# Performance work log

Measured on AMD Instinct MI355X. Metric: run time of the kernel, lower is better.

## Reference

```python
import jax, jax.numpy as jnp
import numpy as np

N_NODES = 50000
N_EDGES = 800000
HIDDEN = 64


def _init_linear(key, fan_in, fan_out):
    kw, kb = jax.random.split(key)
    lim = 1.0 / np.sqrt(fan_in)
    W = jax.random.uniform(kw, (fan_in, fan_out), jnp.float32, -lim, lim)
    b = jax.random.uniform(kb, (fan_out,), jnp.float32, -lim, lim)
    return W, b


def setup_inputs() -> dict:
    key = jax.random.key(0)
    ks = jax.random.split(key, 10)
    feat = jax.random.normal(ks[0], (N_NODES, HIDDEN), jnp.float32)
    x = jax.random.normal(ks[1], (N_NODES, 3), jnp.float32)
    src = jax.random.randint(ks[2], (N_EDGES,), 0, N_NODES, jnp.int32)
    dst = jax.random.randint(ks[3], (N_EDGES,), 0, N_NODES, jnp.int32)
    # message MLP: (2H+1) -> H -> H, relu after both layers (last_activation=mid)
    W1, b1 = _init_linear(ks[4], 2 * HIDDEN + 1, HIDDEN)
    W2, b2 = _init_linear(ks[5], HIDDEN, HIDDEN)
    # soft edge gate: H -> 1
    we, be = _init_linear(ks[6], HIDDEN, 1)
    # update MLP: H -> H -> H, relu mid, no last activation
    U1, c1 = _init_linear(ks[7], HIDDEN, HIDDEN)
    U2, c2 = _init_linear(ks[8], HIDDEN, HIDDEN)
    return dict(feat=feat, x=x, src=src, dst=dst,
                W1=W1, b1=b1, W2=W2, b2=b2, we=we, be=be,
                U1=U1, c1=c1, U2=U2, c2=c2)


def reference(feat, x, src, dst, W1, b1, W2, b2, we, be, U1, c1, U2, c2):
    # per-edge squared distance between endpoint coordinates: [E, 1]
    sqd = jnp.sum((x[src] - x[dst]) ** 2, axis=-1, keepdims=True)
    # message input: [E, 2H+1]
    msg_in = jnp.concatenate([feat[src], feat[dst], sqd], axis=-1)
    # 2-layer message MLP with relu mid and last activation
    m = jax.nn.relu(jax.nn.relu(msg_in @ W1 + b1) @ W2 + b2)
    # sigmoid soft-edge gate: [E, 1]
    gate = jax.nn.sigmoid(m @ we + be)
    # scatter-sum gated messages to destination nodes: [N, H]
    m_sum = jax.ops.segment_sum(m * gate, dst, num_segments=N_NODES)
    # node update MLP on (m_sum + feat), residual add
    h = m_sum + feat
    h_new = jax.nn.relu(h @ U1 + c1) @ U2 + c2
    return h_new + feat
```

## Files before the change

### kernel.cpp

```cpp
#include <hip/hip_runtime.h>
#include <hip/hip_bf16.h>
#include <stdint.h>

#define N_NODES 50000
#define N_EDGES 800000
#define HDIM 64
#define SCAN_N (N_NODES + 1)

#define MSUM_OFF   0
#define EP_OFF     12800000
#define DEG_OFF    (EP_OFF + 12800000)
#define OFFS_OFF   (DEG_OFF + 204800)
#define POS_OFF    (OFFS_OFF + 204800)
#define FB_OFF     (POS_OFF + 204800)
#define W1T_OFF    (FB_OFF + (size_t)N_NODES * HDIM * 2)
#define W2T_OFF    (W1T_OFF + 16384)
#define U1T_OFF    (W2T_OFF + 8192)
#define U2T_OFF    (U1T_OFF + 8192)
#define CST_OFF    (U2T_OFF + 8192)
#define WS_NEED    (CST_OFF + 4096)

#define CVT_BLOCKS   1563
#define PREPW_BLOCKS 82
#define MZ_BLOCKS    3125
#define HIST_BLOCKS  1024

typedef __attribute__((ext_vector_type(8))) short short8;
typedef __attribute__((ext_vector_type(4))) float floatx4;

__device__ __forceinline__ float bf2f(unsigned short u) {
    union { unsigned int i; float f; } v; v.i = ((unsigned int)u) << 16; return v.f;
}
__device__ __forceinline__ unsigned short f2bf(float f) {
    __hip_bfloat16 h = __float2bfloat16(f);
    return *reinterpret_cast<unsigned short*>(&h);
}

__device__ __forceinline__ int detect_is_bf16(const unsigned short* p) {
    int cnt = 0;
    #pragma unroll
    for (int i = 0; i < 64; ++i) {
        unsigned short b = p[i];
        int e = (b >> 7) & 0xFF;
        cnt += ((e >= 97 && e <= 157) || (b & 0x7FFF) == 0) ? 1 : 0;
    }
    return cnt >= 56;
}

__device__ __forceinline__ float getf(const void* p, unsigned int i, int isb) {
    return isb ? bf2f(((const unsigned short*)p)[i]) : ((const float*)p)[i];
}

__device__ __forceinline__ short8 get8bf(const void* p, unsigned int i, int isb) {
    if (isb) {
        return *reinterpret_cast<const short8*>((const short*)p + i);
    } else {
        const float4 f0 = *reinterpret_cast<const float4*>((const float*)p + i);
        const float4 f1 = *reinterpret_cast<const float4*>((const float*)p + i + 4);
        short8 a;
        a[0] = (short)f2bf(f0.x); a[1] = (short)f2bf(f0.y);
        a[2] = (short)f2bf(f0.z); a[3] = (short)f2bf(f0.w);
        a[4] = (short)f2bf(f1.x); a[5] = (short)f2bf(f1.y);
        a[6] = (short)f2bf(f1.z); a[7] = (short)f2bf(f1.w);
        return a;
    }
}

#define COMPILER_FENCE() asm volatile("" ::: "memory")
#define WAIT_LDS() __builtin_amdgcn_s_waitcnt(0xC07F)

__global__ __launch_bounds__(256) void prep_kernel(
    const void* __restrict__ feat, unsigned short* __restrict__ fb,
    const void* __restrict__ W1, const void* __restrict__ W2,
    const void* __restrict__ U1, const void* __restrict__ U2,
    const void* __restrict__ b1, const void* __restrict__ b2,
    const void* __restrict__ we, const void* __restrict__ be,
    unsigned short* __restrict__ w1t, unsigned short* __restrict__ w2t,
    unsigned short* __restrict__ u1t, unsigned short* __restrict__ u2t,
    float* __restrict__ cst,
    const int* __restrict__ dst, int* __restrict__ deg,
    uint4* __restrict__ msumz)
{
    const int b = blockIdx.x;
    if (b < CVT_BLOCKS) {
        const int isb = detect_is_bf16((const unsigned short*)feat);
        int i = (b * 256 + threadIdx.x) * 8;
        if (i >= N_NODES * HDIM) return;
        if (isb) {
            *reinterpret_cast<uint4*>(fb + i) =
                *reinterpret_cast<const uint4*>((const unsigned short*)feat + i);
        } else {
            float4 f0 = *reinterpret_cast<const float4*>((const float*)feat + i);
            float4 f1 = *reinterpret_cast<const float4*>((const float*)feat + i + 4);
            ushort4 a = {f2bf(f0.x), f2bf(f0.y), f2bf(f0.z), f2bf(f0.w)};
            ushort4 c = {f2bf(f1.x), f2bf(f1.y), f2bf(f1.z), f2bf(f1.w)};
            *reinterpret_cast<ushort4*>(fb + i)     = a;
            *reinterpret_cast<ushort4*>(fb + i + 4) = c;
        }
    } else if (b < CVT_BLOCKS + PREPW_BLOCKS) {
        const int isb = detect_is_bf16((const unsigned short*)feat);
        int idx = (b - CVT_BLOCKS) * 256 + threadIdx.x;
        if (idx < 8192) {
            int n = idx >> 7, k = idx & 127;
            w1t[idx] = f2bf(getf(W1, k * 64 + n, isb));
        } else if (idx < 12288) {
            int i = idx - 8192, n = i >> 6, k = i & 63;
            w2t[i] = f2bf(getf(W2, k * 64 + n, isb));
        } else if (idx < 16384) {
            int i = idx - 12288, n = i >> 6, k = i & 63;
            u1t[i] = f2bf(getf(U1, k * 64 + n, isb));
        } else if (idx < 20480) {
            int i = idx - 16384, n = i >> 6, k = i & 63;
            u2t[i] = f2bf(getf(U2, k * 64 + n, isb));
        } else if (idx < 20737) {
            int i = idx - 20480;
            float v;
            if (i < 64)       v = getf(b1, i, isb);
            else if (i < 128) v = getf(W1, 128 * 64 + (i - 64), isb);
            else if (i < 192) v = getf(b2, i - 128, isb);
            else if (i < 256) v = getf(we, i - 192, isb);
            else              v = getf(be, 0, isb);
            cst[i] = v;
        }
    } else if (b < CVT_BLOCKS + PREPW_BLOCKS + MZ_BLOCKS) {
        int i = (b - CVT_BLOCKS - PREPW_BLOCKS) * 256 + threadIdx.x;
        if (i < N_NODES * HDIM / 4)
            msumz[i] = (uint4){0u, 0u, 0u, 0u};
    } else {
        int e0 = (b - CVT_BLOCKS - PREPW_BLOCKS - MZ_BLOCKS) * 256 + threadIdx.x;
        for (int e = e0; e < N_EDGES; e += HIST_BLOCKS * 256)
            atomicAdd(&deg[dst[e]], 1);
    }
}

__global__ void scan1_kernel(const int* __restrict__ deg, int* __restrict__ part) {
    __shared__ int s[1024];
    int g = blockIdx.x * 1024 + threadIdx.x;
    s[threadIdx.x] = (g < SCAN_N) ? deg[g] : 0;
    __syncthreads();
    for (int off = 512; off > 0; off >>= 1) {
        if (threadIdx.x < off) s[threadIdx.x] += s[threadIdx.x + off];
        __syncthreads();
    }
    if (threadIdx.x == 0) part[blockIdx.x] = s[0];
}

__global__ void scan2_kernel(int* __restrict__ part, int nparts) {
    if (threadIdx.x == 0) {
        int run = 0;
        for (int i = 0; i < nparts; ++i) { int t = part[i]; part[i] = run; run += t; }
    }
}

__global__ void scan3_kernel(const int* __restrict__ deg, const int* __restrict__ part,
                             int* __restrict__ offs, int* __restrict__ pos) {
    __shared__ int s[1024];
    int g = blockIdx.x * 1024 + threadIdx.x;
    int v = (g < SCAN_N) ? deg[g] : 0;
    s[threadIdx.x] = v;
    __syncthreads();
    for (int off = 1; off < 1024; off <<= 1) {
        int t = (threadIdx.x >= off) ? s[threadIdx.x - off] : 0;
        __syncthreads();
        s[threadIdx.x] += t;
        __syncthreads();
    }
    int excl = s[threadIdx.x] - v + part[blockIdx.x];
    if (g < SCAN_N) { offs[g] = excl; pos[g] = excl; }
}

__global__ __launch_bounds__(256) void permute_kernel(
    const void* __restrict__ feat, const void* __restrict__ xpos,
    const int* __restrict__ src, const int* __restrict__ dst,
    int* __restrict__ pos, uint4* __restrict__ epack)
{
    const int isb = detect_is_bf16((const unsigned short*)feat);
    int e = blockIdx.x * 256 + threadIdx.x;
    if (e < N_EDGES) {
        int s = src[e], d = dst[e];
        int slot = atomicAdd(&pos[d], 1);
        float dx = getf(xpos, s * 3 + 0, isb) - getf(xpos, d * 3 + 0, isb);
        float dy = getf(xpos, s * 3 + 1, isb) - getf(xpos, d * 3 + 1, isb);
        float dz = getf(xpos, s * 3 + 2, isb) - getf(xpos, d * 3 + 2, isb);
        float sqd = dx * dx + dy * dy + dz * dz;
        uint4 p;
        p.x = (unsigned int)s;
        p.y = (unsigned int)d;
        p.z = __float_as_uint(sqd);
        p.w = 0u;
        epack[slot] = p;
    }
}

template <bool CSR>
__global__ __launch_bounds__(512, 4) void edge_kernel(
    const unsigned short* __restrict__ fbf,
    const unsigned short* __restrict__ w1t, const unsigned short* __restrict__ w2t,
    const float* __restrict__ cst,
    const void* __restrict__ feat, const void* __restrict__ xpos,
    const int* __restrict__ src, const int* __restrict__ dst,
    const uint4* __restrict__ epack,
    const void* __restrict__ W1, const void* __restrict__ b1,
    const void* __restrict__ W2, const void* __restrict__ b2,
    const void* __restrict__ we, const void* __restrict__ be,
    float* __restrict__ msum, unsigned int msum_cap)
{
    __shared__ __align__(16) short sW1[16][64][8];
    __shared__ __align__(16) short sW2[8][64][8];
    __shared__ __align__(16) short sA2[8][16][72];

    const int tid  = threadIdx.x;
    const int wave = tid >> 6;
    const int lane = tid & 63;
    const int l15  = lane & 15;
    const int quad = lane >> 4;
    const int rowb = quad * 4;

    float b1r[4], w1lr[4], b2r[4], wer[4];
    float ber;
    short8 bw1[4][4];
    short8 bw2[2][4];

    if constexpr (CSR) {
        for (int i = tid; i < 16 * 64; i += 512) {
            int f = i >> 6, l = i & 63;
            int n = (f & 3) * 16 + (l & 15);
            int k0 = (f >> 2) * 32 + (l >> 4) * 8;
            *reinterpret_cast<short8*>(&sW1[f][l][0]) =
                *reinterpret_cast<const short8*>(w1t + n * 128 + k0);
        }
        for (int i = tid; i < 8 * 64; i += 512) {
            int f = i >> 6, l = i & 63;
            int n = (f & 3) * 16 + (l & 15);
            int k0 = (f >> 2) * 32 + (l >> 4) * 8;
            *reinterpret_cast<short8*>(&sW2[f][l][0]) =
                *reinterpret_cast<const short8*>(w2t + n * 64 + k0);
        }
        #pragma unroll
        for (int nt = 0; nt < 4; ++nt) {
            int n = nt * 16 + l15;
            b1r[nt]  = cst[n];
            w1lr[nt] = cst[64 + n];
            b2r[nt]  = cst[128 + n];
            wer[nt]  = cst[192 + n];
        }
        ber = cst[256];
        __syncthreads();

        const int nbiter = N_EDGES / 256;
        for (int it = blockIdx.x; it < nbiter; it += gridDim.x) {
            const int ebase = it * 256 + wave * 16;

            int sidx = 0, didx = 0;
            float sqd = 0.f;
            if (lane < 32) {
                int e = ebase + l15 + ((lane >> 4) << 7);
                uint4 p = epack[e];
                sidx = (int)p.x;
                didx = (int)p.y;
                sqd  = __uint_as_float(p.z);
            }
            const int snA = __shfl(sidx, l15);
            const int dnA = __shfl(didx, l15);
            const int snB = __shfl(sidx, l15 + 16);
            const int dnB = __shfl(didx, l15 + 16);

            short8 caA[4], caB[4];
            #pragma unroll
            for (int c = 0; c < 4; ++c) {
                const int nA = (c < 2) ? snA : dnA;
                const int nB = (c < 2) ? snB : dnB;
                caA[c] = *reinterpret_cast<const short8*>(
                    (const short*)fbf + (unsigned int)nA * 64u + (c & 1) * 32 + quad * 8);
                caB[c] = *reinterpret_cast<const short8*>(
                    (const short*)fbf + (unsigned int)nB * 64u + (c & 1) * 32 + quad * 8);
            }

            floatx4 accA[4], accB[4];
            #pragma unroll
            for (int nt = 0; nt < 4; ++nt) {
                accA[nt] = (floatx4){0.f, 0.f, 0.f, 0.f};
                accB[nt] = (floatx4){0.f, 0.f, 0.f, 0.f};
            }
            #pragma unroll
            for (int c = 0; c < 4; ++c) {
                #pragma unroll
                for (int nt = 0; nt < 4; ++nt) {
                    short8 wb = *reinterpret_cast<const short8*>(&sW1[c * 4 + nt][lane][0]);
                    accA[nt] = __builtin_amdgcn_mfma_f32_16x16x32_bf16(caA[c], wb, accA[nt], 0, 0, 0);
                    accB[nt] = __builtin_amdgcn_mfma_f32_16x16x32_bf16(caB[c], wb, accB[nt], 0, 0, 0);
                }
            }

            float sqA[4], sqB[4];
            #pragma unroll
            for (int r = 0; r < 4; ++r) {
                sqA[r] = __shfl(sqd, rowb + r);
                sqB[r] = __shfl(sqd, 16 + rowb + r);
            }

            #pragma unroll
            for (int nt = 0; nt < 4; ++nt)
                #pragma unroll
                for (int r = 0; r < 4; ++r) {
                    float vA = fmaxf(fmaf(sqA[r], w1lr[nt], accA[nt][r]) + b1r[nt], 0.f);
                    sA2[wave][rowb + r][nt * 16 + l15] = (short)f2bf(vA);
                }
            COMPILER_FENCE();
            WAIT_LDS();

            floatx4 acc2A[4];
            #pragma unroll
            for (int nt = 0; nt < 4; ++nt) acc2A[nt] = (floatx4){0.f, 0.f, 0.f, 0.f};
            #pragma unroll
            for (int c = 0; c < 2; ++c) {
                short8 aA = *reinterpret_cast<const short8*>(&sA2[wave][l15][c * 32 + quad * 8]);
                #pragma unroll
                for (int nt = 0; nt < 4; ++nt) {
                    short8 wb = *reinterpret_cast<const short8*>(&sW2[c * 4 + nt][lane][0]);
                    acc2A[nt] = __builtin_amdgcn_mfma_f32_16x16x32_bf16(aA, wb, acc2A[nt], 0, 0, 0);
                }
            }
            COMPILER_FENCE();
            WAIT_LDS();

            #pragma unroll
            for (int nt = 0; nt < 4; ++nt)
                #pragma unroll
                for (int r = 0; r < 4; ++r) {
                    float vB = fmaxf(fmaf(sqB[r], w1lr[nt], accB[nt][r]) + b1r[nt], 0.f);
                    sA2[wave][rowb + r][nt * 16 + l15] = (short)f2bf(vB);
                }
            COMPILER_FENCE();
            WAIT_LDS();

            floatx4 acc2B[4];
            #pragma unroll
            for (int nt = 0; nt < 4; ++nt) acc2B[nt] = (floatx4){0.f, 0.f, 0.f, 0.f};
            #pragma unroll
            for (int c = 0; c < 2; ++c) {
                short8 aB = *reinterpret_cast<const short8*>(&sA2[wave][l15][c * 32 + quad * 8]);
                #pragma unroll
                for (int nt = 0; nt < 4; ++nt) {
                    short8 wb = *reinterpret_cast<const short8*>(&sW2[c * 4 + nt][lane][0]);
                    acc2B[nt] = __builtin_amdgcn_mfma_f32_16x16x32_bf16(aB, wb, acc2B[nt], 0, 0, 0);
                }
            }
            COMPILER_FENCE();

            float mvA[4][4], mvB[4][4];
            float pA[4] = {0.f, 0.f, 0.f, 0.f};
            float pB[4] = {0.f, 0.f, 0.f, 0.f};
            #pragma unroll
            for (int nt = 0; nt < 4; ++nt)
                #pragma unroll
                for (int r = 0; r < 4; ++r) {
                    float vA = fmaxf(acc2A[nt][r] + b2r[nt], 0.f);
                    float vB = fmaxf(acc2B[nt][r] + b2r[nt], 0.f);
                    mvA[nt][r] = vA;
                    mvB[nt][r] = vB;
                    pA[r] = fmaf(vA, wer[nt], pA[r]);
                    pB[r] = fmaf(vB, wer[nt], pB[r]);
                }
            #pragma unroll
            for (int off = 1; off < 16; off <<= 1)
                #pragma unroll
                for (int r = 0; r < 4; ++r) {
                    pA[r] += __shfl_xor(pA[r], off);
                    pB[r] += __shfl_xor(pB[r], off);
                }
            float gA[4], gB[4];
            #pragma unroll
            for (int r = 0; r < 4; ++r) {
                gA[r] = 1.f / (1.f + __expf(-(pA[r] + ber)));
                gB[r] = 1.f / (1.f + __expf(-(pB[r] + ber)));
            }

            int grp = (lane >> 4) & 1;
            int nd = __shfl(didx, grp * 16 + ((l15 + 1) & 15));
            int flag = (lane < 32) && ((l15 == 15) || (nd != didx));
            unsigned long long bal = __ballot(flag);
            unsigned int mA = (unsigned int)(bal & 0xFFFFull);
            unsigned int mB = (unsigned int)((bal >> 16) & 0xFFFFull);

            int lo = 0;
            while (mA) {
                int hi = __ffs(mA) - 1;
                float s0 = 0.f, s1 = 0.f, s2 = 0.f, s3 = 0.f;
                #pragma unroll
                for (int r = 0; r < 4; ++r) {
                    int gr = rowb + r;
                    float g = (gr >= lo && gr <= hi) ? gA[r] : 0.f;
                    s0 = fmaf(g, mvA[0][r], s0);
                    s1 = fmaf(g, mvA[1][r], s1);
                    s2 = fmaf(g, mvA[2][r], s2);
                    s3 = fmaf(g, mvA[3][r], s3);
                }
                s0 += __shfl_xor(s0, 16); s0 += __shfl_xor(s0, 32);
                s1 += __shfl_xor(s1, 16); s1 += __shfl_xor(s1, 32);
                s2 += __shfl_xor(s2, 16); s2 += __shfl_xor(s2, 32);
                s3 += __shfl_xor(s3, 16); s3 += __shfl_xor(s3, 32);
                int d = __shfl(didx, hi);
                float v = (quad == 0) ? s0 : (quad == 1) ? s1 : (quad == 2) ? s2 : s3;
                unsafeAtomicAdd(&msum[(unsigned int)d * 64u + (unsigned int)quad * 16u + l15], v);
                lo = hi + 1;
                mA &= mA - 1;
            }
            lo = 0;
            while (mB) {
                int hi = __ffs(mB) - 1;
                float s0 = 0.f, s1 = 0.f, s2 = 0.f, s3 = 0.f;
                #pragma unroll
                for (int r = 0; r < 4; ++r) {
                    int gr = rowb + r;
                    float g = (gr >= lo && gr <= hi) ? gB[r] : 0.f;
                    s0 = fmaf(g, mvB[0][r], s0);
                    s1 = fmaf(g, mvB[1][r], s1);
                    s2 = fmaf(g, mvB[2][r], s2);
                    s3 = fmaf(g, mvB[3][r], s3);
                }
                s0 += __shfl_xor(s0, 16); s0 += __shfl_xor(s0, 32);
                s1 += __shfl_xor(s1, 16); s1 += __shfl_xor(s1, 32);
                s2 += __shfl_xor(s2, 16); s2 += __shfl_xor(s2, 32);
                s3 += __shfl_xor(s3, 16); s3 += __shfl_xor(s3, 32);
                int d = __shfl(didx, 16 + hi);
                float v = (quad == 0) ? s0 : (quad == 1) ? s1 : (quad == 2) ? s2 : s3;
                unsafeAtomicAdd(&msum[(unsigned int)d * 64u + (unsigned int)quad * 16u + l15], v);
                lo = hi + 1;
                mB &= mB - 1;
            }
        }
    } else {
        const int isb = detect_is_bf16((const unsigned short*)feat);
        #pragma unroll
        for (int c = 0; c < 4; ++c)
            #pragma unroll
            for (int nt = 0; nt < 4; ++nt) {
                short8 b;
                #pragma unroll
                for (int j = 0; j < 8; ++j)
                    b[j] = (short)f2bf(getf(W1, (c * 32 + quad * 8 + j) * 64 + nt * 16 + l15, isb));
                bw1[c][nt] = b;
            }
        #pragma unroll
        for (int c = 0; c < 2; ++c)
            #pragma unroll
            for (int nt = 0; nt < 4; ++nt) {
                short8 b;
                #pragma unroll
                for (int j = 0; j < 8; ++j)
                    b[j] = (short)f2bf(getf(W2, (c * 32 + quad * 8 + j) * 64 + nt * 16 + l15, isb));
                bw2[c][nt] = b;
            }
        #pragma unroll
        for (int nt = 0; nt < 4; ++nt) {
            int n = nt * 16 + l15;
            b1r[nt]  = getf(b1, n, isb);
            w1lr[nt] = getf(W1, 128 * 64 + n, isb);
            b2r[nt]  = getf(b2, n, isb);
            wer[nt]  = getf(we, n, isb);
        }
        ber = getf(be, 0, isb);

        const int ntiles = N_EDGES / 128;
        for (int t = blockIdx.x; t < ntiles; t += gridDim.x) {
            const int ebase = t * 128 + wave * 16;
            int sidx = 0, didx = 0;
            float sqd = 0.f;
            if (lane < 16) {
                int e = ebase + lane;
                sidx = src[e];
                didx = dst[e];
                float dx = getf(xpos, sidx * 3 + 0, isb) - getf(xpos, didx * 3 + 0, isb);
                float dy = getf(xpos, sidx * 3 + 1, isb) - getf(xpos, didx * 3 + 1, isb);
                float dz = getf(xpos, sidx * 3 + 2, isb) - getf(xpos, didx * 3 + 2, isb);
                sqd = dx * dx + dy * dy + dz * dz;
            }
            const int sn     = __shfl(sidx, l15);
            const int dn_row = __shfl(didx, l15);

            floatx4 acc[4];
            #pragma unroll
            for (int nt = 0; nt < 4; ++nt) acc[nt] = (floatx4){0.f, 0.f, 0.f, 0.f};
            #pragma unroll
            for (int c = 0; c < 4; ++c) {
                const int node = (c < 2) ? sn : dn_row;
                const unsigned int aoff = (unsigned int)node * 64u + (c & 1) * 32 + quad * 8;
                short8 a = get8bf(feat, aoff, isb);
                #pragma unroll
                for (int nt = 0; nt < 4; ++nt)
                    acc[nt] = __builtin_amdgcn_mfma_f32_16x16x32_bf16(a, bw1[c][nt], acc[nt], 0, 0, 0);
            }

            float sq[4];
            #pragma unroll
            for (int r = 0; r < 4; ++r) sq[r] = __shfl(sqd, rowb + r);
            #pragma unroll
            for (int nt = 0; nt < 4; ++nt)
                #pragma unroll
                for (int r = 0; r < 4; ++r) {
                    float v = fmaxf(acc[nt][r] + b1r[nt] + sq[r] * w1lr[nt], 0.f);
                    sA2[wave][rowb + r][nt * 16 + l15] = (short)f2bf(v);
                }
            COMPILER_FENCE();
            WAIT_LDS();

            floatx4 acc2[4];
            #pragma unroll
            for (int nt = 0; nt < 4; ++nt) acc2[nt] = (floatx4){0.f, 0.f, 0.f, 0.f};
            #pragma unroll
            for (int c = 0; c < 2; ++c) {
                short8 a = *reinterpret_cast<const short8*>(&sA2[wave][l15][c * 32 + quad * 8]);
                #pragma unroll
                for (int nt = 0; nt < 4; ++nt)
                    acc2[nt] = __builtin_amdgcn_mfma_f32_16x16x32_bf16(a, bw2[c][nt], acc2[nt], 0, 0, 0);
            }
            COMPILER_FENCE();
            WAIT_LDS();

            float mval[4][4];
            float part[4] = {0.f, 0.f, 0.f, 0.f};
            #pragma unroll
            for (int nt = 0; nt < 4; ++nt)
                #pragma unroll
                for (int r = 0; r < 4; ++r) {
                    float v = fmaxf(acc2[nt][r] + b2r[nt], 0.f);
                    mval[nt][r] = v;
                    part[r] += v * wer[nt];
                }
            #pragma unroll
            for (int off = 1; off < 16; off <<= 1)
                #pragma unroll
                for (int r = 0; r < 4; ++r) part[r] += __shfl_xor(part[r], off);
            float gate[4];
            #pragma unroll
            for (int r = 0; r < 4; ++r)
                gate[r] = 1.f / (1.f + __expf(-(part[r] + ber)));

            #pragma unroll
            for (int r = 0; r < 4; ++r) {
                int dn = __shfl(didx, rowb + r);
                unsigned int base = (unsigned int)dn * 64u;
                if (base + 64u <= msum_cap) {
                    #pragma unroll
                    for (int nt = 0; nt < 4; ++nt)
                        unsafeAtomicAdd(&msum[base + nt * 16 + l15], mval[nt][r] * gate[r]);
                }
            }
        }
    }
}

__global__ __launch_bounds__(256, 2) void node_kernel(
    const float* __restrict__ msum,
    const unsigned short* __restrict__ u1t, const unsigned short* __restrict__ u2t,
    const void* __restrict__ feat,
    const void* __restrict__ U1, const void* __restrict__ c1v,
    const void* __restrict__ U2, const void* __restrict__ c2v,
    void* __restrict__ out)
{
    __shared__ __align__(16) short sT[4][16][72];
    __shared__ __align__(16) float sF[4][16][68];

    const int isb  = detect_is_bf16((const unsigned short*)feat);
    const int tid  = threadIdx.x;
    const int wave = tid >> 6;
    const int lane = tid & 63;
    const int l15  = lane & 15;
    const int quad = lane >> 4;

    short8 u1f[2][4], u2f[2][4];
    if (u1t) {
        #pragma unroll
        for (int nt = 0; nt < 4; ++nt) {
            const int n = nt * 16 + l15;
            #pragma unroll
            for (int c = 0; c < 2; ++c) {
                u1f[c][nt] = *reinterpret_cast<const short8*>(u1t + n * 64 + c * 32 + quad * 8);
                u2f[c][nt] = *reinterpret_cast<const short8*>(u2t + n * 64 + c * 32 + quad * 8);
            }
        }
    } else {
        #pragma unroll
        for (int c = 0; c < 2; ++c)
            #pragma unroll
            for (int nt = 0; nt < 4; ++nt) {
                short8 a, b;
                #pragma unroll
                for (int j = 0; j < 8; ++j) {
                    int k = c * 32 + quad * 8 + j, n = nt * 16 + l15;
                    a[j] = (short)f2bf(getf(U1, k * 64 + n, isb));
                    b[j] = (short)f2bf(getf(U2, k * 64 + n, isb));
                }
                u1f[c][nt] = a; u2f[c][nt] = b;
            }
    }
    float c1r[4], c2r[4];
    #pragma unroll
    for (int nt = 0; nt < 4; ++nt) {
        c1r[nt] = getf(c1v, nt * 16 + l15, isb);
        c2r[nt] = getf(c2v, nt * 16 + l15, isb);
    }
    const int rowb = quad * 4;

    const int ntile = (N_NODES + 15) / 16;
    const int t = blockIdx.x * 4 + wave;
    if (t < ntile) {
        const int node = t * 16 + l15;

        short8 ah[2];
        #pragma unroll
        for (int c = 0; c < 2; ++c) {
            unsigned int off = (unsigned int)node * 64u + c * 32 + quad * 8;
            float4 m0 = *reinterpret_cast<const float4*>(msum + off);
            float4 m1 = *reinterpret_cast<const float4*>(msum + off + 4);
            float mv[8] = {m0.x, m0.y, m0.z, m0.w, m1.x, m1.y, m1.z, m1.w};
            float hv[8];
            if (isb) {
                short8 fv = *reinterpret_cast<const short8*>((const short*)feat + off);
                #pragma unroll
                for (int j = 0; j < 8; ++j) hv[j] = bf2f((unsigned short)fv[j]);
            } else {
                float4 f0 = *reinterpret_cast<const float4*>((const float*)feat + off);
                float4 f1 = *reinterpret_cast<const float4*>((const float*)feat + off + 4);
                hv[0] = f0.x; hv[1] = f0.y; hv[2] = f0.z; hv[3] = f0.w;
                hv[4] = f1.x; hv[5] = f1.y; hv[6] = f1.z; hv[7] = f1.w;
            }
            short8 a;
            #pragma unroll
            for (int j = 0; j < 8; ++j) a[j] = (short)f2bf(mv[j] + hv[j]);
            ah[c] = a;
        }

        floatx4 acc[4];
        #pragma unroll
        for (int nt = 0; nt < 4; ++nt) acc[nt] = (floatx4){0.f, 0.f, 0.f, 0.f};
        #pragma unroll
        for (int c = 0; c < 2; ++c)
            #pragma unroll
            for (int nt = 0; nt < 4; ++nt)
                acc[nt] = __builtin_amdgcn_mfma_f32_16x16x32_bf16(ah[c], u1f[c][nt], acc[nt], 0, 0, 0);

        #pragma unroll
        for (int nt = 0; nt < 4; ++nt)
            #pragma unroll
            for (int r = 0; r < 4; ++r) {
                float v = fmaxf(acc[nt][r] + c1r[nt], 0.f);
                sT[wave][rowb + r][nt * 16 + l15] = (short)f2bf(v);
            }
        COMPILER_FENCE();
        WAIT_LDS();

        floatx4 acc2[4];
        #pragma unroll
        for (int nt = 0; nt < 4; ++nt) acc2[nt] = (floatx4){0.f, 0.f, 0.f, 0.f};
        #pragma unroll
        for (int c = 0; c < 2; ++c) {
            short8 a = *reinterpret_cast<const short8*>(&sT[wave][l15][c * 32 + quad * 8]);
            #pragma unroll
            for (int nt = 0; nt < 4; ++nt)
                acc2[nt] = __builtin_amdgcn_mfma_f32_16x16x32_bf16(a, u2f[c][nt], acc2[nt], 0, 0, 0);
        }
        COMPILER_FENCE();

        #pragma unroll
        for (int nt = 0; nt < 4; ++nt)
            #pragma unroll
            for (int r = 0; r < 4; ++r)
                sF[wave][rowb + r][nt * 16 + l15] = acc2[nt][r] + c2r[nt];
        COMPILER_FENCE();
        WAIT_LDS();

        const unsigned int ob = (unsigned int)node * 64u + quad * 16;
        if (isb) {
            const unsigned short* fp = (const unsigned short*)feat + ob;
            unsigned short* op = (unsigned short*)out + ob;
            #pragma unroll
            for (int k = 0; k < 2; ++k) {
                ushort4 o0, o1;
                float4 v0 = *reinterpret_cast<const float4*>(&sF[wave][l15][quad * 16 + k * 8]);
                float4 v1 = *reinterpret_cast<const float4*>(&sF[wave][l15][quad * 16 + k * 8 + 4]);
                const ushort4 f0 = *reinterpret_cast<const ushort4*>(fp + k * 8);
                const ushort4 f1 = *reinterpret_cast<const ushort4*>(fp + k * 8 + 4);
                o0.x = f2bf(v0.x + bf2f(f0.x)); o0.y = f2bf(v0.y + bf2f(f0.y));
                o0.z = f2bf(v0.z + bf2f(f0.z)); o0.w = f2bf(v0.w + bf2f(f0.w));
                o1.x = f2bf(v1.x + bf2f(f1.x)); o1.y = f2bf(v1.y + bf2f(f1.y));
                o1.z = f2bf(v1.z + bf2f(f1.z)); o1.w = f2bf(v1.w + bf2f(f1.w));
                *reinterpret_cast<ushort4*>(op + k * 8)     = o0;
                *reinterpret_cast<ushort4*>(op + k * 8 + 4) = o1;
            }
        } else {
            const float* fp = (const float*)feat + ob;
            float* op = (float*)out + ob;
            #pragma unroll
            for (int k = 0; k < 4; ++k) {
                float4 v = *reinterpret_cast<const float4*>(&sF[wave][l15][quad * 16 + k * 4]);
                float4 f = *reinterpret_cast<const float4*>(fp + k * 4);
                float4 o = {v.x + f.x, v.y + f.y, v.z + f.z, v.w + f.w};
                *reinterpret_cast<float4*>(op + k * 4) = o;
            }
        }
        COMPILER_FENCE();
    }
}

extern "C" void kernel_launch(void* const* d_in, const int* in_sizes, int n_in,
                              void* d_out, int out_size, void* d_ws, size_t ws_size,
                              hipStream_t stream) {
    const void* feat = d_in[0];
    const void* x    = d_in[1];
    const int* src   = (const int*)d_in[2];
    const int* dst   = (const int*)d_in[3];
    const void* W1   = d_in[4];
    const void* b1   = d_in[5];
    const void* W2   = d_in[6];
    const void* b2   = d_in[7];
    const void* we   = d_in[8];
    const void* be   = d_in[9];
    const void* U1   = d_in[10];
    const void* c1   = d_in[11];
    const void* U2   = d_in[12];
    const void* c2   = d_in[13];
    char* ws = (char*)d_ws;

    if (ws_size >= WS_NEED) {
        float* msum = (float*)(ws + MSUM_OFF);
        uint4* epack = (uint4*)(ws + EP_OFF);
        int* deg  = (int*)(ws + DEG_OFF);
        int* offs = (int*)(ws + OFFS_OFF);
        int* pos  = (int*)(ws + POS_OFF);
        unsigned short* fb  = (unsigned short*)(ws + FB_OFF);
        unsigned short* w1t = (unsigned short*)(ws + W1T_OFF);
        unsigned short* w2t = (unsigned short*)(ws + W2T_OFF);
        unsigned short* u1t = (unsigned short*)(ws + U1T_OFF);
        unsigned short* u2t = (unsigned short*)(ws + U2T_OFF);
        float* cst = (float*)(ws + CST_OFF);

        hipMemsetAsync(deg, 0, 204800, stream);
        prep_kernel<<<CVT_BLOCKS + PREPW_BLOCKS + MZ_BLOCKS + HIST_BLOCKS, 256, 0, stream>>>(
            feat, fb, W1, W2, U1, U2, b1, b2, we, be,
            w1t, w2t, u1t, u2t, cst, dst, deg, (uint4*)msum);
        scan1_kernel<<<49, 1024, 0, stream>>>(deg, offs + 51200 - 64);
        scan2_kernel<<<1, 64, 0, stream>>>(offs + 51200 - 64, 49);
        scan3_kernel<<<49, 1024, 0, stream>>>(deg, offs + 51200 - 64, offs, pos);
        permute_kernel<<<(N_EDGES + 255) / 256, 256, 0, stream>>>(feat, x, src, dst, pos, epack);
        edge_kernel<true><<<768, 512, 0, stream>>>(fb, w1t, w2t, cst, feat, x, src, dst, epack,
                                                   W1, b1, W2, b2, we, be,
                                                   msum, (unsigned int)(N_NODES * HDIM));
        node_kernel<<<((N_NODES + 15) / 16 + 3) / 4, 256, 0, stream>>>(
            msum, u1t, u2t, feat, U1, c1, U2, c2, d_out);
    } else {
        float* msum = (float*)ws;
        size_t need = (size_t)N_NODES * HDIM * sizeof(float);
        size_t clr  = need < ws_size ? need : ws_size;
        unsigned int cap = (unsigned int)(ws_size / sizeof(float));
        if (cap > (unsigned int)(N_NODES * HDIM)) cap = (unsigned int)(N_NODES * HDIM);

        hipMemsetAsync(msum, 0, clr, stream);
        edge_kernel<false><<<1250, 512, 0, stream>>>(nullptr, nullptr, nullptr, nullptr,
                                                     feat, x, src, dst,
                                                     nullptr, W1, b1, W2, b2, we, be,
                                                     msum, cap);
        node_kernel<<<((N_NODES + 15) / 16 + 3) / 4, 256, 0, stream>>>(
            msum, nullptr, nullptr, feat, U1, c1, U2, c2, d_out);
    }
}
```

Measured before the change: 268.8 us.

## Fold scan phases, memset msum, double-buffer LDS, use contiguous edge chunks per block

```diff
diff --git a/kernel.cpp b/kernel.cpp
--- a/kernel.cpp
+++ b/kernel.cpp
@@ -8,11 +8,13 @@
 #define SCAN_N (N_NODES + 1)
 
 #define MSUM_OFF   0
-#define EP_OFF     12800000
-#define DEG_OFF    (EP_OFF + 12800000)
-#define OFFS_OFF   (DEG_OFF + 204800)
+#define DEG_OFF    12800000
+#define ZERO_BYTES (DEG_OFF + 204800)
+#define PART_OFF   (DEG_OFF + 204800)
+#define OFFS_OFF   (PART_OFF + 1024)
 #define POS_OFF    (OFFS_OFF + 204800)
-#define FB_OFF     (POS_OFF + 204800)
+#define EP_OFF     (POS_OFF + 204800)
+#define FB_OFF     (EP_OFF + 12800000)
 #define W1T_OFF    (FB_OFF + (size_t)N_NODES * HDIM * 2)
 #define W2T_OFF    (W1T_OFF + 16384)
 #define U1T_OFF    (W2T_OFF + 8192)
@@ -22,7 +24,6 @@
 
 #define CVT_BLOCKS   1563
 #define PREPW_BLOCKS 82
-#define MZ_BLOCKS    3125
 #define HIST_BLOCKS  1024
 
 typedef __attribute__((ext_vector_type(8))) short short8;
@@ -78,8 +79,7 @@
     unsigned short* __restrict__ w1t, unsigned short* __restrict__ w2t,
     unsigned short* __restrict__ u1t, unsigned short* __restrict__ u2t,
     float* __restrict__ cst,
-    const int* __restrict__ dst, int* __restrict__ deg,
-    uint4* __restrict__ msumz)
+    const int* __restrict__ dst, int* __restrict__ deg)
 {
     const int b = blockIdx.x;
     if (b < CVT_BLOCKS) {
@@ -122,12 +122,8 @@
             else              v = getf(be, 0, isb);
             cst[i] = v;
         }
-    } else if (b < CVT_BLOCKS + PREPW_BLOCKS + MZ_BLOCKS) {
-        int i = (b - CVT_BLOCKS - PREPW_BLOCKS) * 256 + threadIdx.x;
-        if (i < N_NODES * HDIM / 4)
-            msumz[i] = (uint4){0u, 0u, 0u, 0u};
     } else {
-        int e0 = (b - CVT_BLOCKS - PREPW_BLOCKS - MZ_BLOCKS) * 256 + threadIdx.x;
+        int e0 = (b - CVT_BLOCKS - PREPW_BLOCKS) * 256 + threadIdx.x;
         for (int e = e0; e < N_EDGES; e += HIST_BLOCKS * 256)
             atomicAdd(&deg[dst[e]], 1);
     }
@@ -145,16 +141,16 @@
     if (threadIdx.x == 0) part[blockIdx.x] = s[0];
 }
 
-__global__ void scan2_kernel(int* __restrict__ part, int nparts) {
-    if (threadIdx.x == 0) {
-        int run = 0;
-        for (int i = 0; i < nparts; ++i) { int t = part[i]; part[i] = run; run += t; }
-    }
-}
-
 __global__ void scan3_kernel(const int* __restrict__ deg, const int* __restrict__ part,
                              int* __restrict__ offs, int* __restrict__ pos) {
     __shared__ int s[1024];
+    __shared__ int sbase;
+    if (threadIdx.x < 64) {
+        int v = (threadIdx.x < blockIdx.x) ? part[threadIdx.x] : 0;
+        #pragma unroll
+        for (int off = 32; off >= 1; off >>= 1) v += __shfl_xor(v, off);
+        if (threadIdx.x == 0) sbase = v;
+    }
     int g = blockIdx.x * 1024 + threadIdx.x;
     int v = (g < SCAN_N) ? deg[g] : 0;
     s[threadIdx.x] = v;
@@ -165,7 +161,7 @@
         s[threadIdx.x] += t;
         __syncthreads();
     }
-    int excl = s[threadIdx.x] - v + part[blockIdx.x];
+    int excl = s[threadIdx.x] - v + sbase;
     if (g < SCAN_N) { offs[g] = excl; pos[g] = excl; }
 }
 
@@ -207,7 +203,7 @@
 {
     __shared__ __align__(16) short sW1[16][64][8];
     __shared__ __align__(16) short sW2[8][64][8];
-    __shared__ __align__(16) short sA2[8][16][72];
+    __shared__ __align__(16) short sA2[2][8][16][72];
 
     const int tid  = threadIdx.x;
     const int wave = tid >> 6;
@@ -248,7 +244,10 @@
         __syncthreads();
 
         const int nbiter = N_EDGES / 256;
-        for (int it = blockIdx.x; it < nbiter; it += gridDim.x) {
+        const int per = (nbiter + (int)gridDim.x - 1) / (int)gridDim.x;
+        const int t0 = blockIdx.x * per;
+        const int t1 = (t0 + per < nbiter) ? t0 + per : nbiter;
+        for (int it = t0; it < t1; ++it) {
             const int ebase = it * 256 + wave * 16;
 
             int sidx = 0, didx = 0;
@@ -298,51 +297,32 @@
                 sqA[r] = __shfl(sqd, rowb + r);
                 sqB[r] = __shfl(sqd, 16 + rowb + r);
             }
-
             #pragma unroll
             for (int nt = 0; nt < 4; ++nt)
                 #pragma unroll
                 for (int r = 0; r < 4; ++r) {
                     float vA = fmaxf(fmaf(sqA[r], w1lr[nt], accA[nt][r]) + b1r[nt], 0.f);
-                    sA2[wave][rowb + r][nt * 16 + l15] = (short)f2bf(vA);
+                    float vB = fmaxf(fmaf(sqB[r], w1lr[nt], accB[nt][r]) + b1r[nt], 0.f);
+                    sA2[0][wave][rowb + r][nt * 16 + l15] = (short)f2bf(vA);
+                    sA2[1][wave][rowb + r][nt * 16 + l15] = (short)f2bf(vB);
                 }
             COMPILER_FENCE();
             WAIT_LDS();
 
-            floatx4 acc2A[4];
-            #pragma unroll
-            for (int nt = 0; nt < 4; ++nt) acc2A[nt] = (floatx4){0.f, 0.f, 0.f, 0.f};
+            floatx4 acc2A[4], acc2B[4];
+            #pragma unroll
+            for (int nt = 0; nt < 4; ++nt) {
+                acc2A[nt] = (floatx4){0.f, 0.f, 0.f, 0.f};
+                acc2B[nt] = (floatx4){0.f, 0.f, 0.f, 0.f};
+            }
             #pragma unroll
             for (int c = 0; c < 2; ++c) {
-                short8 aA = *reinterpret_cast<const short8*>(&sA2[wave][l15][c * 32 + quad * 8]);
+                short8 aA = *reinterpret_cast<const short8*>(&sA2[0][wave][l15][c * 32 + quad * 8]);
+                short8 aB = *reinterpret_cast<const short8*>(&sA2[1][wave][l15][c * 32 + quad * 8]);
                 #pragma unroll
                 for (int nt = 0; nt < 4; ++nt) {
                     short8 wb = *reinterpret_cast<const short8*>(&sW2[c * 4 + nt][lane][0]);
                     acc2A[nt] = __builtin_amdgcn_mfma_f32_16x16x32_bf16(aA, wb, acc2A[nt], 0, 0, 0);
-                }
-            }
-            COMPILER_FENCE();
-            WAIT_LDS();
-
-            #pragma unroll
-            for (int nt = 0; nt < 4; ++nt)
-                #pragma unroll
-                for (int r = 0; r < 4; ++r) {
-                    float vB = fmaxf(fmaf(sqB[r], w1lr[nt], accB[nt][r]) + b1r[nt], 0.f);
-                    sA2[wave][rowb + r][nt * 16 + l15] = (short)f2bf(vB);
-                }
-            COMPILER_FENCE();
-            WAIT_LDS();
-
-            floatx4 acc2B[4];
-            #pragma unroll
-            for (int nt = 0; nt < 4; ++nt) acc2B[nt] = (floatx4){0.f, 0.f, 0.f, 0.f};
-            #pragma unroll
-            for (int c = 0; c < 2; ++c) {
-                short8 aB = *reinterpret_cast<const short8*>(&sA2[wave][l15][c * 32 + quad * 8]);
-                #pragma unroll
-                for (int nt = 0; nt < 4; ++nt) {
-                    short8 wb = *reinterpret_cast<const short8*>(&sW2[c * 4 + nt][lane][0]);
                     acc2B[nt] = __builtin_amdgcn_mfma_f32_16x16x32_bf16(aB, wb, acc2B[nt], 0, 0, 0);
                 }
             }
@@ -500,7 +480,7 @@
                 #pragma unroll
                 for (int r = 0; r < 4; ++r) {
                     float v = fmaxf(acc[nt][r] + b1r[nt] + sq[r] * w1lr[nt], 0.f);
-                    sA2[wave][rowb + r][nt * 16 + l15] = (short)f2bf(v);
+                    sA2[0][wave][rowb + r][nt * 16 + l15] = (short)f2bf(v);
                 }
             COMPILER_FENCE();
             WAIT_LDS();
@@ -510,7 +490,7 @@
             for (int nt = 0; nt < 4; ++nt) acc2[nt] = (floatx4){0.f, 0.f, 0.f, 0.f};
             #pragma unroll
             for (int c = 0; c < 2; ++c) {
-                short8 a = *reinterpret_cast<const short8*>(&sA2[wave][l15][c * 32 + quad * 8]);
+                short8 a = *reinterpret_cast<const short8*>(&sA2[0][wave][l15][c * 32 + quad * 8]);
                 #pragma unroll
                 for (int nt = 0; nt < 4; ++nt)
                     acc2[nt] = __builtin_amdgcn_mfma_f32_16x16x32_bf16(a, bw2[c][nt], acc2[nt], 0, 0, 0);
@@ -725,10 +705,11 @@
 
     if (ws_size >= WS_NEED) {
         float* msum = (float*)(ws + MSUM_OFF);
-        uint4* epack = (uint4*)(ws + EP_OFF);
         int* deg  = (int*)(ws + DEG_OFF);
+        int* part = (int*)(ws + PART_OFF);
         int* offs = (int*)(ws + OFFS_OFF);
         int* pos  = (int*)(ws + POS_OFF);
+        uint4* epack = (uint4*)(ws + EP_OFF);
         unsigned short* fb  = (unsigned short*)(ws + FB_OFF);
         unsigned short* w1t = (unsigned short*)(ws + W1T_OFF);
         unsigned short* w2t = (unsigned short*)(ws + W2T_OFF);
@@ -736,15 +717,14 @@
         unsigned short* u2t = (unsigned short*)(ws + U2T_OFF);
         float* cst = (float*)(ws + CST_OFF);
 
-        hipMemsetAsync(deg, 0, 204800, stream);
-        prep_kernel<<<CVT_BLOCKS + PREPW_BLOCKS + MZ_BLOCKS + HIST_BLOCKS, 256, 0, stream>>>(
+        hipMemsetAsync(ws, 0, ZERO_BYTES, stream);
+        prep_kernel<<<CVT_BLOCKS + PREPW_BLOCKS + HIST_BLOCKS, 256, 0, stream>>>(
             feat, fb, W1, W2, U1, U2, b1, b2, we, be,
-            w1t, w2t, u1t, u2t, cst, dst, deg, (uint4*)msum);
-        scan1_kernel<<<49, 1024, 0, stream>>>(deg, offs + 51200 - 64);
-        scan2_kernel<<<1, 64, 0, stream>>>(offs + 51200 - 64, 49);
-        scan3_kernel<<<49, 1024, 0, stream>>>(deg, offs + 51200 - 64, offs, pos);
+            w1t, w2t, u1t, u2t, cst, dst, deg);
+        scan1_kernel<<<49, 1024, 0, stream>>>(deg, part);
+        scan3_kernel<<<49, 1024, 0, stream>>>(deg, part, offs, pos);
         permute_kernel<<<(N_EDGES + 255) / 256, 256, 0, stream>>>(feat, x, src, dst, pos, epack);
-        edge_kernel<true><<<768, 512, 0, stream>>>(fb, w1t, w2t, cst, feat, x, src, dst, epack,
+        edge_kernel<true><<<625, 512, 0, stream>>>(fb, w1t, w2t, cst, feat, x, src, dst, epack,
                                                    W1, b1, W2, b2, we, be,
                                                    msum, (unsigned int)(N_NODES * HDIM));
         node_kernel<<<((N_NODES + 15) / 16 + 3) / 4, 256, 0, stream>>>(
```

After: 257.4 us. 1.04x faster.
